# Kernel tuning notes

Hardware: AMD Instinct MI355X
Metric: run time of the kernel (lower is better)

Reference implementation:

```python
import jax, jax.numpy as jnp
import numpy as np


def _log_g(x):
    # log of g(x) = where(x>=0, x+0.5, sigmoid(x)), computed stably in log-space
    return jnp.where(x >= 0, jnp.log(jax.nn.relu(x) + 0.5), -jax.nn.softplus(-x))


def _mingru_layer(h, w_hg_l, w_out_l, rms_w_l):
    # h: [B,T,H]; w_hg_l: [2*DI,H]; w_out_l: [H,DI]; rms_w_l: [H]
    hg = jnp.einsum('bth,dh->btd', h, w_hg_l)          # [B,T,2*DI]
    hidden, gate = jnp.split(hg, 2, axis=-1)            # each [B,T,DI]
    log_coeffs = -jax.nn.softplus(gate)                 # log a_t
    log_values = -jax.nn.softplus(-gate) + _log_g(hidden)  # log(z_t * g(h~_t))
    # Heinsen log-space associative scan (prev_hidden = 0, contributes nothing)
    a_star = jnp.cumsum(log_coeffs, axis=1)
    log_h = a_star + jax.lax.cumlogsumexp(log_values - a_star, axis=1)
    out = jnp.exp(log_h)                                # [B,T,DI]
    out = jnp.einsum('btd,hd->bth', out, w_out_l) + h   # proj_out + residual
    eps = jnp.finfo(out.dtype).eps
    out = out * jax.lax.rsqrt(jnp.mean(out * out, axis=-1, keepdims=True) + eps)
    return out * rms_w_l


def setup_inputs() -> dict:
    key = jax.random.key(0)
    ks = jax.random.split(key, 6)
    B, T, OBS, H, DI, L, A = 32, 1024, 512, 512, 1024, 2, 16
    s = 0.05  # weight scale keeps softplus/exp chain well-conditioned
    return {
        'x': jax.random.normal(ks[0], (B, T, OBS), jnp.float32),
        'enc_w': s * jax.random.normal(ks[1], (H, OBS), jnp.float32),
        'enc_b': jnp.zeros((H,), jnp.float32),
        'w_hg': s * jax.random.normal(ks[2], (L, 2 * DI, H), jnp.float32),
        'w_out': s * jax.random.normal(ks[3], (L, H, DI), jnp.float32),
        'rms_w': jnp.ones((L, H), jnp.float32),
        'dec_w': s * jax.random.normal(ks[4], (A, H), jnp.float32),
        'dec_b': jnp.zeros((A,), jnp.float32),
        'val_w': s * jax.random.normal(ks[5], (1, H), jnp.float32),
        'val_b': jnp.zeros((1,), jnp.float32),
    }


def reference(x, enc_w, enc_b, w_hg, w_out, rms_w, dec_w, dec_b, val_w, val_b):
    B, T, _ = x.shape
    # encoder: Linear + exact gelu
    h = jax.nn.gelu(jnp.einsum('bto,ho->bth', x, enc_w) + enc_b, approximate=False)
    for l in range(w_hg.shape[0]):
        h = _mingru_layer(h, w_hg[l], w_out[l], rms_w[l])
    flat = h.reshape(B * T, -1)
    logits = flat @ dec_w.T + dec_b                     # [B*T, A]
    values = (flat @ val_w.T + val_b).reshape(B, T)
    return logits, values
```

## Files before the change

### kernel.cpp

```cpp
#include <hip/hip_runtime.h>
#include <math.h>

#define MROWS 32768
#define T_LEN 1024

typedef __attribute__((ext_vector_type(8))) short bf16x8;
typedef __attribute__((ext_vector_type(4))) float f32x4;

__device__ __forceinline__ unsigned short f2bf(float f) {
  union { float f; unsigned u; } x; x.f = f;
  unsigned r = x.u + 0x7fffu + ((x.u >> 16) & 1u);
  return (unsigned short)(r >> 16);
}
__device__ __forceinline__ float bf2f(unsigned short u) {
  union { unsigned u; float f; } x; x.u = ((unsigned)u) << 16; return x.f;
}

__device__ __forceinline__ void gload_lds16(const void* g, void* l) {
  __builtin_amdgcn_global_load_lds(
      (const __attribute__((address_space(1))) void*)g,
      (__attribute__((address_space(3))) void*)l, 16, 0, 0);
}

__device__ __forceinline__ float sigm_neg(float x) {
  return __builtin_amdgcn_rcpf(1.0f + __expf(x));
}

#define VMCNT2 asm volatile("s_waitcnt vmcnt(2)" ::: "memory")
#define VMCNT0 asm volatile("s_waitcnt vmcnt(0)" ::: "memory")
#define LGKM0 do { asm volatile("s_waitcnt lgkmcnt(0)" ::: "memory"); \
                   __builtin_amdgcn_sched_barrier(0); } while (0)
#define BAR __builtin_amdgcn_s_barrier()

template<int MODE>
__global__ __launch_bounds__(256, 2)
void gemm_bt(const unsigned short* __restrict__ A, int lda,
             const unsigned short* __restrict__ B,
             int N, int K,
             const float* __restrict__ bias,
             const unsigned short* res,
             unsigned short* outb)
{
  __shared__ __align__(16) unsigned short sA[128 * 64];
  __shared__ __align__(16) unsigned short sB[128 * 64];
  const int tid  = threadIdx.x;
  const int wave = tid >> 6, lane = tid & 63;
  const int lid = blockIdx.x;
  const int swz = (lid & 7) * ((int)gridDim.x >> 3) + (lid >> 3);
  const int m0 = (swz >> 2) * 128;
  const int n0 = (swz & 3) * 128;
  const int srow   = lane >> 3;
  const int sslotb = ((lane & 7) ^ srow) * 16;
  const int wm = wave & 1, wn = wave >> 1;
  const int r16 = lane & 15, q = lane >> 4;

  f32x4 acc[4][4];
#pragma unroll
  for (int i = 0; i < 4; i++)
#pragma unroll
    for (int j = 0; j < 4; j++)
#pragma unroll
      for (int e = 0; e < 4; e++) acc[i][j][e] = 0.0f;

  const char* Ab = (const char*)A;
  const char* Bb = (const char*)B;
  char* sAb = (char*)sA;
  char* sBb = (char*)sB;

  for (int kt = 0; kt < K; kt += 64) {
#pragma unroll
    for (int i = 0; i < 4; i++) {
      const int j = wave * 4 + i;
      const int row = j * 8 + srow;
      gload_lds16(Ab + ((size_t)(m0 + row) * lda + kt) * 2 + sslotb, sAb + j * 1024);
      gload_lds16(Bb + ((size_t)(n0 + row) * K   + kt) * 2 + sslotb, sBb + j * 1024);
    }
    __syncthreads();
#pragma unroll
    for (int kh = 0; kh < 2; kh++) {
      bf16x8 af[4], bfr[4];
#pragma unroll
      for (int mt = 0; mt < 4; mt++) {
        const int row = wm * 64 + mt * 16 + r16;
        af[mt] = *(const bf16x8*)(sAb + row * 128 + ((((kh << 2) | q) ^ (row & 7)) * 16));
      }
#pragma unroll
      for (int nt = 0; nt < 4; nt++) {
        const int row = wn * 64 + nt * 16 + r16;
        bfr[nt] = *(const bf16x8*)(sBb + row * 128 + ((((kh << 2) | q) ^ (row & 7)) * 16));
      }
#pragma unroll
      for (int mt = 0; mt < 4; mt++)
#pragma unroll
        for (int nt = 0; nt < 4; nt++)
          acc[mt][nt] = __builtin_amdgcn_mfma_f32_16x16x32_bf16(af[mt], bfr[nt], acc[mt][nt], 0, 0, 0);
    }
    __syncthreads();
  }

#pragma unroll
  for (int mt = 0; mt < 4; mt++) {
#pragma unroll
    for (int nt = 0; nt < 4; nt++) {
#pragma unroll
      for (int r = 0; r < 4; r++) {
        const int m = m0 + wm * 64 + mt * 16 + q * 4 + r;
        const int n = n0 + wn * 64 + nt * 16 + r16;
        const size_t idx = (size_t)m * N + n;
        float v = acc[mt][nt][r];
        if (MODE == 0) {
          v += bias[n];
          v = 0.5f * v * (1.0f + erff(v * 0.70710678118654752f));
        } else if (MODE == 2) {
          v += bf2f(res[idx]);
        }
        outb[idx] = f2bf(v);
      }
    }
  }
}

__global__ __launch_bounds__(512, 2)
void gemm_hg8(const unsigned short* __restrict__ A,
              const unsigned short* __restrict__ B,
              unsigned short* __restrict__ outb)
{
  __shared__ __align__(16) char smem[131072];
  const int tid  = threadIdx.x;
  const int wave = tid >> 6, lane = tid & 63;
  const int lid = blockIdx.x;
  const int swz = (lid & 7) * 128 + (lid >> 3);
  const int m0  = (swz >> 3) * 256;
  const int nh0 = (swz & 7) * 128;
  const int wm = wave >> 2, wn = wave & 3;
  const int r16 = lane & 15, q4 = lane >> 4;

  const int srow   = tid >> 3;
  const int sslotb = ((tid & 7) ^ (srow & 7)) * 16;
  const int sldso  = tid * 16;

  const int slot0 = ((q4)     ^ (r16 & 7)) * 16;
  const int slot1 = ((4 | q4) ^ (r16 & 7)) * 16;

  const char* Ab = (const char*)A;
  const char* Bb = (const char*)B;

  f32x4 acc[8][4];
#pragma unroll
  for (int i = 0; i < 8; i++)
#pragma unroll
    for (int j = 0; j < 4; j++)
#pragma unroll
      for (int e = 0; e < 4; e++) acc[i][j][e] = 0.0f;

  auto stage2 = [&](int u, int qp) {
    char* base = smem + (u & 1) * 65536;
    const int kt2 = u << 7;
#pragma unroll
    for (int i = 0; i < 2; ++i) {
      const int qq = qp * 2 + i;
      if (qq < 4) {
        gload_lds16(Ab + (size_t)(m0 + qq * 64 + srow) * 1024 + kt2 + sslotb,
                    base + qq * 8192 + sldso);
      } else if (qq < 6) {
        gload_lds16(Bb + (size_t)(nh0 + (qq - 4) * 64 + srow) * 1024 + kt2 + sslotb,
                    base + 32768 + (qq - 4) * 8192 + sldso);
      } else {
        gload_lds16(Bb + (size_t)(1024 + nh0 + (qq - 6) * 64 + srow) * 1024 + kt2 + sslotb,
                    base + 49152 + (qq - 6) * 8192 + sldso);
      }
    }
  };

  auto lda_frags = [&](const char* base, int kh, int mh,
                       bf16x8 af[4], bf16x8 bh[2], bf16x8 bg[2]) {
    const int slot = kh ? slot1 : slot0;
#pragma unroll
    for (int mt = 0; mt < 4; ++mt) {
      const int row = wm * 128 + mh * 64 + mt * 16 + r16;
      af[mt] = *(const bf16x8*)(base + row * 128 + slot);
    }
#pragma unroll
    for (int nt = 0; nt < 2; ++nt) {
      const int row = wn * 32 + nt * 16 + r16;
      bh[nt] = *(const bf16x8*)(base + 32768 + row * 128 + slot);
      bg[nt] = *(const bf16x8*)(base + 49152 + row * 128 + slot);
    }
  };

  auto mfma16 = [&](int mh, bf16x8 af[4], bf16x8 bh[2], bf16x8 bg[2]) {
    __builtin_amdgcn_s_setprio(1);
#pragma unroll
    for (int mt = 0; mt < 4; ++mt) {
      const int MT = mh * 4 + mt;
      acc[MT][0] = __builtin_amdgcn_mfma_f32_16x16x32_bf16(af[mt], bh[0], acc[MT][0], 0, 0, 0);
      acc[MT][1] = __builtin_amdgcn_mfma_f32_16x16x32_bf16(af[mt], bh[1], acc[MT][1], 0, 0, 0);
      acc[MT][2] = __builtin_amdgcn_mfma_f32_16x16x32_bf16(af[mt], bg[0], acc[MT][2], 0, 0, 0);
      acc[MT][3] = __builtin_amdgcn_mfma_f32_16x16x32_bf16(af[mt], bg[1], acc[MT][3], 0, 0, 0);
    }
    __builtin_amdgcn_s_setprio(0);
  };

#pragma unroll
  for (int qp = 0; qp < 4; ++qp) stage2(0, qp);
  VMCNT0; BAR;

  for (int t = 0; t < 4; ++t) {
    const int u1 = 2 * t + 1;
    const char* b0 = smem;
    const char* b1 = smem + 65536;
    bf16x8 af[4], bh[2], bg[2];
    const bool more = (t < 3);

#pragma unroll
    for (int pi = 0; pi < 4; ++pi) {
      const int kh = pi >> 1, mh = pi & 1;
      if (pi == 0) {
        stage2(u1, 0);
        VMCNT2;
        BAR;
        lda_frags(b0, kh, mh, af, bh, bg);
      } else {
        lda_frags(b0, kh, mh, af, bh, bg);
        stage2(u1, pi);
        BAR;
      }
      LGKM0;
      mfma16(mh, af, bh, bg);
      BAR;
    }

#pragma unroll
    for (int pi = 0; pi < 4; ++pi) {
      const int kh = pi >> 1, mh = pi & 1;
      if (pi == 0) {
        if (more) { stage2(u1 + 1, 0); VMCNT2; } else { VMCNT0; }
        BAR;
        lda_frags(b1, kh, mh, af, bh, bg);
      } else {
        lda_frags(b1, kh, mh, af, bh, bg);
        if (more) stage2(u1 + 1, pi);
        BAR;
      }
      LGKM0;
      mfma16(mh, af, bh, bg);
      BAR;
    }
  }

#pragma unroll
  for (int MT = 0; MT < 8; ++MT) {
#pragma unroll
    for (int nf = 0; nf < 2; ++nf) {
#pragma unroll
      for (int r = 0; r < 4; ++r) {
        const int m = m0 + wm * 128 + MT * 16 + q4 * 4 + r;
        const int d = nh0 + wn * 32 + nf * 16 + r16;
        const float vh = acc[MT][nf][r];
        const float vg = acc[MT][nf + 2][r];
        const float G = (vh >= 0.0f) ? (vh + 0.5f) : sigm_neg(-vh);
        const float a = sigm_neg(vg);
        const float b = (1.0f - a) * G;
        const size_t base = (size_t)m * 2048 + d;
        outb[base]        = f2bf(b);
        outb[base + 1024] = f2bf(a);
      }
    }
  }
}

__global__ __launch_bounds__(256)
void scan_kernel(unsigned short* hg) {
  __shared__ unsigned long long sAB[256 * 16];
  __shared__ float sA[16 * 32];
  __shared__ float sH[16 * 32];
  const int b  = blockIdx.x >> 5;
  const int dg = blockIdx.x & 31;
  const int tid = threadIdx.x;
  const int c  = tid >> 4;
  const int dp = tid & 15;
  unsigned int* base = (unsigned int*)(hg + (size_t)b * T_LEN * 2048);
  const int du = dg * 16 + dp;

  float carry = 0.0f;

  for (int seg = 0; seg < 4; ++seg) {
    const int t0 = seg * 256 + c * 16;

    float A0 = 1.0f, A1 = 1.0f, h0 = 0.0f, h1 = 0.0f;
#pragma unroll
    for (int tl = 0; tl < 16; ++tl) {
      const int t = t0 + tl;
      const unsigned bpk = base[t * 1024 + du];
      const unsigned apk = base[t * 1024 + 512 + du];
      sAB[(c * 16 + tl) * 16 + dp] =
          (unsigned long long)apk | ((unsigned long long)bpk << 32);
      const float fa0 = bf2f((unsigned short)apk), fa1 = bf2f((unsigned short)(apk >> 16));
      const float fb0 = bf2f((unsigned short)bpk), fb1 = bf2f((unsigned short)(bpk >> 16));
      A0 *= fa0; h0 = fa0 * h0 + fb0;
      A1 *= fa1; h1 = fa1 * h1 + fb1;
    }
    sA[c * 32 + 2 * dp] = A0;  sA[c * 32 + 2 * dp + 1] = A1;
    sH[c * 32 + 2 * dp] = h0;  sH[c * 32 + 2 * dp + 1] = h1;
    __syncthreads();

    if (tid < 32) {
      float hin = carry;
#pragma unroll
      for (int cc = 0; cc < 16; ++cc) {
        const float a  = sA[cc * 32 + tid];
        const float hs = sH[cc * 32 + tid];
        sA[cc * 32 + tid] = hin;
        hin = hs + a * hin;
      }
      carry = hin;
    }
    __syncthreads();

    float hh0 = sA[c * 32 + 2 * dp];
    float hh1 = sA[c * 32 + 2 * dp + 1];
#pragma unroll
    for (int tl = 0; tl < 16; ++tl) {
      const int t = t0 + tl;
      const unsigned long long ab = sAB[(c * 16 + tl) * 16 + dp];
      const float fa0 = bf2f((unsigned short)ab);
      const float fa1 = bf2f((unsigned short)(ab >> 16));
      const float fb0 = bf2f((unsigned short)(ab >> 32));
      const float fb1 = bf2f((unsigned short)(ab >> 48));
      hh0 = fa0 * hh0 + fb0;
      hh1 = fa1 * hh1 + fb1;
      base[t * 1024 + 512 + du] = (unsigned)f2bf(hh0) | ((unsigned)f2bf(hh1) << 16);
    }
    __syncthreads();
  }
}

__global__ __launch_bounds__(256)
void rms_kernel(unsigned short* __restrict__ hb, const float* __restrict__ w) {
  const int wid  = (blockIdx.x * blockDim.x + threadIdx.x) >> 6;
  const int lane = threadIdx.x & 63;
  unsigned short* row = hb + (size_t)wid * 512;
  float v[8];
  float ss = 0.0f;
#pragma unroll
  for (int j = 0; j < 8; j++) { v[j] = bf2f(row[lane + 64 * j]); ss += v[j] * v[j]; }
#pragma unroll
  for (int off = 32; off >= 1; off >>= 1) ss += __shfl_xor(ss, off, 64);
  const float r = rsqrtf(ss * (1.0f / 512.0f) + 1.1920929e-7f);
#pragma unroll
  for (int j = 0; j < 8; j++) {
    const int k = lane + 64 * j;
    row[k] = f2bf(v[j] * r * w[k]);
  }
}

__global__ __launch_bounds__(256)
void rms_dec_kernel(const unsigned short* __restrict__ hb,
                    const float* __restrict__ w,
                    const float* __restrict__ dec_w,
                    const float* __restrict__ dec_b,
                    const float* __restrict__ val_w,
                    const float* __restrict__ val_b,
                    float* __restrict__ out) {
  const int row  = (blockIdx.x * blockDim.x + threadIdx.x) >> 6;
  const int lane = threadIdx.x & 63;
  const unsigned short* hr = hb + (size_t)row * 512;
  float v[8];
  float ss = 0.0f;
#pragma unroll
  for (int j = 0; j < 8; j++) { v[j] = bf2f(hr[lane + 64 * j]); ss += v[j] * v[j]; }
#pragma unroll
  for (int off = 32; off >= 1; off >>= 1) ss += __shfl_xor(ss, off, 64);
  const float r = rsqrtf(ss * (1.0f / 512.0f) + 1.1920929e-7f);

  float acc[17];
#pragma unroll
  for (int a = 0; a < 17; a++) acc[a] = 0.0f;
#pragma unroll
  for (int j = 0; j < 8; j++) {
    const int k = lane + 64 * j;
    const float hv = v[j] * r * w[k];
#pragma unroll
    for (int a = 0; a < 16; a++) acc[a] += hv * dec_w[a * 512 + k];
    acc[16] += hv * val_w[k];
  }
#pragma unroll
  for (int a = 0; a < 17; a++) {
#pragma unroll
    for (int off = 32; off >= 1; off >>= 1) acc[a] += __shfl_xor(acc[a], off, 64);
  }
  if (lane == 0) {
    float* logits = out;
    float* values = out + (size_t)MROWS * 16;
#pragma unroll
    for (int a = 0; a < 16; a++) logits[(size_t)row * 16 + a] = acc[a] + dec_b[a];
    values[row] = acc[16] + val_b[0];
  }
}

__global__ __launch_bounds__(256)
void conv_all(const float* __restrict__ x, const float* __restrict__ enc_w,
              const float* __restrict__ w_hg, const float* __restrict__ w_out,
              unsigned short* __restrict__ xb, unsigned short* __restrict__ wenc,
              unsigned short* __restrict__ whg, unsigned short* __restrict__ wout) {
  const int i = blockIdx.x * 256 + threadIdx.x;
  const float* src; unsigned short* dst; int off;
  if (i < 4194304)      { src = x;     dst = xb;   off = i; }
  else if (i < 4259840) { src = enc_w; dst = wenc; off = i - 4194304; }
  else if (i < 4784128) { src = w_hg;  dst = whg;  off = i - 4259840; }
  else                  { src = w_out; dst = wout; off = i - 4784128; }
  const float4 v = ((const float4*)src)[off];
  const unsigned long long pack =
      (unsigned long long)f2bf(v.x) |
      ((unsigned long long)f2bf(v.y) << 16) |
      ((unsigned long long)f2bf(v.z) << 32) |
      ((unsigned long long)f2bf(v.w) << 48);
  ((unsigned long long*)dst)[off] = pack;
}

extern "C" void kernel_launch(void* const* d_in, const int* in_sizes, int n_in,
                              void* d_out, int out_size, void* d_ws, size_t ws_size,
                              hipStream_t stream) {
  const float* x     = (const float*)d_in[0];
  const float* enc_w = (const float*)d_in[1];
  const float* enc_b = (const float*)d_in[2];
  const float* w_hg  = (const float*)d_in[3];
  const float* w_out = (const float*)d_in[4];
  const float* rms_w = (const float*)d_in[5];
  const float* dec_w = (const float*)d_in[6];
  const float* dec_b = (const float*)d_in[7];
  const float* val_w = (const float*)d_in[8];
  const float* val_b = (const float*)d_in[9];
  float* out = (float*)d_out;

  if (ws_size < 174587904u) return;

  char* ws = (char*)d_ws;
  unsigned short* hg   = (unsigned short*)(ws);
  unsigned short* xb   = (unsigned short*)(ws);
  unsigned short* hb   = (unsigned short*)(ws + 134217728);
  unsigned short* wenc = (unsigned short*)(ws + 167772160);
  unsigned short* whg  = wenc + 262144;
  unsigned short* wout = whg + 2097152;

  conv_all<<<19712, 256, 0, stream>>>(x, enc_w, w_hg, w_out, xb, wenc, whg, wout);

  gemm_bt<0><<<1024, 256, 0, stream>>>(xb, 512, wenc, 512, 512, enc_b, nullptr, hb);

  for (int l = 0; l < 2; ++l) {
    gemm_hg8<<<1024, 512, 0, stream>>>(hb, whg + (size_t)l * 1048576, hg);
    scan_kernel<<<1024, 256, 0, stream>>>(hg);
    gemm_bt<2><<<1024, 256, 0, stream>>>(hg + 1024, 2048, wout + (size_t)l * 524288,
                                         512, 1024, nullptr, hb, hb);
    if (l == 0) rms_kernel<<<8192, 256, 0, stream>>>(hb, rms_w);
  }

  rms_dec_kernel<<<8192, 256, 0, stream>>>(hb, rms_w + 512, dec_w, dec_b,
                                           val_w, val_b, out);
}
```

Measured before the change: 585.8 us.

## Replace N=512 GEMMs with double-buffered 256x128 tile, 8-wave pipelined kernel

Replaces the single-buffered 128x128 gemm_bt used for the encoder and output projections with a 512-thread kernel. It computes 256x128 tiles and double-buffers LDS (96KB), so global-to-LDS loads for the next K tile overlap MFMA work on the current one. It also uses split-phase staging with vmcnt waits and s_setprio around the MFMA bursts. The grid halves to 512 blocks and N is hardcoded to 512. The large LDS footprint limits occupancy, and K must be a multiple of 128.

```diff
diff --git a/kernel.cpp b/kernel.cpp
--- a/kernel.cpp
+++ b/kernel.cpp
@@ -26,6 +26,7 @@
   return __builtin_amdgcn_rcpf(1.0f + __expf(x));
 }
 
+#define VMCNT3 asm volatile("s_waitcnt vmcnt(3)" ::: "memory")
 #define VMCNT2 asm volatile("s_waitcnt vmcnt(2)" ::: "memory")
 #define VMCNT0 asm volatile("s_waitcnt vmcnt(0)" ::: "memory")
 #define LGKM0 do { asm volatile("s_waitcnt lgkmcnt(0)" ::: "memory"); \
@@ -33,80 +34,131 @@
 #define BAR __builtin_amdgcn_s_barrier()
 
 template<int MODE>
-__global__ __launch_bounds__(256, 2)
-void gemm_bt(const unsigned short* __restrict__ A, int lda,
-             const unsigned short* __restrict__ B,
-             int N, int K,
-             const float* __restrict__ bias,
-             const unsigned short* res,
-             unsigned short* outb)
+__global__ __launch_bounds__(512, 2)
+void gemm_512_8(const unsigned short* __restrict__ A, int lda,
+                const unsigned short* __restrict__ B, int K,
+                const float* __restrict__ bias,
+                const unsigned short* res,
+                unsigned short* __restrict__ outb)
 {
-  __shared__ __align__(16) unsigned short sA[128 * 64];
-  __shared__ __align__(16) unsigned short sB[128 * 64];
+  __shared__ __align__(16) char smem[98304];
   const int tid  = threadIdx.x;
   const int wave = tid >> 6, lane = tid & 63;
   const int lid = blockIdx.x;
-  const int swz = (lid & 7) * ((int)gridDim.x >> 3) + (lid >> 3);
-  const int m0 = (swz >> 2) * 128;
+  const int swz = (lid & 7) * 64 + (lid >> 3);
+  const int m0 = (swz >> 2) * 256;
   const int n0 = (swz & 3) * 128;
-  const int srow   = lane >> 3;
-  const int sslotb = ((lane & 7) ^ srow) * 16;
-  const int wm = wave & 1, wn = wave >> 1;
-  const int r16 = lane & 15, q = lane >> 4;
-
-  f32x4 acc[4][4];
-#pragma unroll
-  for (int i = 0; i < 4; i++)
-#pragma unroll
-    for (int j = 0; j < 4; j++)
-#pragma unroll
-      for (int e = 0; e < 4; e++) acc[i][j][e] = 0.0f;
+  const int wm = wave >> 1, wn = wave & 1;
+  const int r16 = lane & 15, q4 = lane >> 4;
+
+  const int srow   = tid >> 3;
+  const int schunk = (tid & 7) ^ (srow & 7);
+  const int sldso  = tid * 16;
+
+  const int slot0 = ((q4)     ^ (r16 & 7)) * 16;
+  const int slot1 = ((4 | q4) ^ (r16 & 7)) * 16;
 
   const char* Ab = (const char*)A;
   const char* Bb = (const char*)B;
-  char* sAb = (char*)sA;
-  char* sBb = (char*)sB;
-
-  for (int kt = 0; kt < K; kt += 64) {
-#pragma unroll
-    for (int i = 0; i < 4; i++) {
-      const int j = wave * 4 + i;
-      const int row = j * 8 + srow;
-      gload_lds16(Ab + ((size_t)(m0 + row) * lda + kt) * 2 + sslotb, sAb + j * 1024);
-      gload_lds16(Bb + ((size_t)(n0 + row) * K   + kt) * 2 + sslotb, sBb + j * 1024);
-    }
-    __syncthreads();
-#pragma unroll
-    for (int kh = 0; kh < 2; kh++) {
-      bf16x8 af[4], bfr[4];
-#pragma unroll
-      for (int mt = 0; mt < 4; mt++) {
-        const int row = wm * 64 + mt * 16 + r16;
-        af[mt] = *(const bf16x8*)(sAb + row * 128 + ((((kh << 2) | q) ^ (row & 7)) * 16));
-      }
-#pragma unroll
-      for (int nt = 0; nt < 4; nt++) {
-        const int row = wn * 64 + nt * 16 + r16;
-        bfr[nt] = *(const bf16x8*)(sBb + row * 128 + ((((kh << 2) | q) ^ (row & 7)) * 16));
-      }
-#pragma unroll
-      for (int mt = 0; mt < 4; mt++)
-#pragma unroll
-        for (int nt = 0; nt < 4; nt++)
-          acc[mt][nt] = __builtin_amdgcn_mfma_f32_16x16x32_bf16(af[mt], bfr[nt], acc[mt][nt], 0, 0, 0);
-    }
-    __syncthreads();
-  }
-
-#pragma unroll
-  for (int mt = 0; mt < 4; mt++) {
-#pragma unroll
-    for (int nt = 0; nt < 4; nt++) {
-#pragma unroll
-      for (int r = 0; r < 4; r++) {
-        const int m = m0 + wm * 64 + mt * 16 + q * 4 + r;
+  const int NT = K >> 6;
+
+  f32x4 acc[4][4];
+#pragma unroll
+  for (int i = 0; i < 4; i++)
+#pragma unroll
+    for (int j = 0; j < 4; j++)
+#pragma unroll
+      for (int e = 0; e < 4; e++) acc[i][j][e] = 0.0f;
+
+  auto stage3 = [&](int u, int half) {
+    char* base = smem + (u & 1) * 49152;
+    const int kt = u << 6;
+#pragma unroll
+    for (int i = 0; i < 3; ++i) {
+      const int qq = half * 3 + i;
+      if (qq < 4) {
+        gload_lds16(Ab + ((size_t)(m0 + qq * 64 + srow) * lda + kt) * 2 + schunk * 16,
+                    base + qq * 8192 + sldso);
+      } else {
+        gload_lds16(Bb + ((size_t)(n0 + (qq - 4) * 64 + srow) * K + kt) * 2 + schunk * 16,
+                    base + 32768 + (qq - 4) * 8192 + sldso);
+      }
+    }
+  };
+
+  auto lda_frags = [&](const char* base, int kh, bf16x8 af[4], bf16x8 bfr[4]) {
+    const int slot = kh ? slot1 : slot0;
+#pragma unroll
+    for (int mt = 0; mt < 4; ++mt) {
+      const int row = wm * 64 + mt * 16 + r16;
+      af[mt] = *(const bf16x8*)(base + row * 128 + slot);
+    }
+#pragma unroll
+    for (int nt = 0; nt < 4; ++nt) {
+      const int row = wn * 64 + nt * 16 + r16;
+      bfr[nt] = *(const bf16x8*)(base + 32768 + row * 128 + slot);
+    }
+  };
+
+  auto mfma16 = [&](bf16x8 af[4], bf16x8 bfr[4]) {
+    __builtin_amdgcn_s_setprio(1);
+#pragma unroll
+    for (int mt = 0; mt < 4; ++mt)
+#pragma unroll
+      for (int nt = 0; nt < 4; ++nt)
+        acc[mt][nt] = __builtin_amdgcn_mfma_f32_16x16x32_bf16(af[mt], bfr[nt], acc[mt][nt], 0, 0, 0);
+    __builtin_amdgcn_s_setprio(0);
+  };
+
+  stage3(0, 0); stage3(0, 1);
+  VMCNT0; BAR;
+
+  for (int t = 0; t < (NT >> 1); ++t) {
+    const int u1 = 2 * t + 1;
+    const char* b0 = smem;
+    const char* b1 = smem + 49152;
+    bf16x8 af[4], bfr[4];
+    const bool more = (t < (NT >> 1) - 1);
+
+    stage3(u1, 0);
+    VMCNT3;
+    BAR;
+    lda_frags(b0, 0, af, bfr);
+    LGKM0;
+    mfma16(af, bfr);
+    BAR;
+
+    lda_frags(b0, 1, af, bfr);
+    stage3(u1, 1);
+    BAR;
+    LGKM0;
+    mfma16(af, bfr);
+    BAR;
+
+    if (more) { stage3(u1 + 1, 0); VMCNT3; } else { VMCNT0; }
+    BAR;
+    lda_frags(b1, 0, af, bfr);
+    LGKM0;
+    mfma16(af, bfr);
+    BAR;
+
+    lda_frags(b1, 1, af, bfr);
+    if (more) stage3(u1 + 1, 1);
+    BAR;
+    LGKM0;
+    mfma16(af, bfr);
+    BAR;
+  }
+
+#pragma unroll
+  for (int mt = 0; mt < 4; ++mt) {
+#pragma unroll
+    for (int nt = 0; nt < 4; ++nt) {
+#pragma unroll
+      for (int r = 0; r < 4; ++r) {
+        const int m = m0 + wm * 64 + mt * 16 + q4 * 4 + r;
         const int n = n0 + wn * 64 + nt * 16 + r16;
-        const size_t idx = (size_t)m * N + n;
+        const size_t idx = (size_t)m * 512 + n;
         float v = acc[mt][nt][r];
         if (MODE == 0) {
           v += bias[n];
@@ -445,13 +497,13 @@
 
   conv_all<<<19712, 256, 0, stream>>>(x, enc_w, w_hg, w_out, xb, wenc, whg, wout);
 
-  gemm_bt<0><<<1024, 256, 0, stream>>>(xb, 512, wenc, 512, 512, enc_b, nullptr, hb);
+  gemm_512_8<0><<<512, 512, 0, stream>>>(xb, 512, wenc, 512, enc_b, nullptr, hb);
 
   for (int l = 0; l < 2; ++l) {
     gemm_hg8<<<1024, 512, 0, stream>>>(hb, whg + (size_t)l * 1048576, hg);
     scan_kernel<<<1024, 256, 0, stream>>>(hg);
-    gemm_bt<2><<<1024, 256, 0, stream>>>(hg + 1024, 2048, wout + (size_t)l * 524288,
-                                         512, 1024, nullptr, hb, hb);
+    gemm_512_8<2><<<512, 512, 0, stream>>>(hg + 1024, 2048, wout + (size_t)l * 524288,
+                                           1024, nullptr, hb, hb);
     if (l == 0) rms_kernel<<<8192, 256, 0, stream>>>(hb, rms_w);
   }
 
```

New measurement: 611.9 us. +4.4%, slower.
